# Kernel optimization log

Measured on AMD Instinct MI355X. Metric: run time of the kernel, lower is better.

Reference implementation:

```python
import jax, jax.numpy as jnp
import numpy as np

B, T, C, H = 2, 2048, 1024, 16
D = C // H  # head_dim = 64


def setup_inputs() -> dict:
    key = jax.random.key(0)
    ks = jax.random.split(key, 5)
    s = 1.0 / np.sqrt(C)
    return {
        "x": jax.random.normal(ks[0], (B, T, C), jnp.float32),
        "Wq": jax.random.normal(ks[1], (C, C), jnp.float32) * s,
        "bq": jnp.zeros((C,), jnp.float32),
        "Wk": jax.random.normal(ks[2], (C, C), jnp.float32) * s,
        "bk": jnp.zeros((C,), jnp.float32),
        "Wv": jax.random.normal(ks[3], (C, C), jnp.float32) * s,
        "bv": jnp.zeros((C,), jnp.float32),
        "Wo": jax.random.normal(ks[4], (C, C), jnp.float32) * s,
        "bo": jnp.zeros((C,), jnp.float32),
    }


def reference(x, Wq, bq, Wk, bk, Wv, bv, Wo, bo):
    Bx, Tx, Cx = x.shape
    # torch Linear: y = x @ W.T + b
    q = (x @ Wq.T + bq).reshape(Bx, Tx, H, D).transpose(0, 2, 1, 3)  # [B,H,T,D]
    k = (x @ Wk.T + bk).reshape(Bx, Tx, H, D).transpose(0, 2, 1, 3)
    v = (x @ Wv.T + bv).reshape(Bx, Tx, H, D).transpose(0, 2, 1, 3)
    att = jnp.einsum("bhqd,bhkd->bhqk", q, k) / np.sqrt(D).astype(np.float32)
    mask = jnp.tril(jnp.ones((Tx, Tx), bool))  # causal mask [T,T]
    att = jnp.where(mask, att, -jnp.inf)
    att = jax.nn.softmax(att, axis=-1)
    out = jnp.einsum("bhqk,bhkd->bhqd", att, v)
    out = out.transpose(0, 2, 1, 3).reshape(Bx, Tx, Cx)
    return out @ Wo.T + bo
```

## Files before the change

kernel.cpp:

```cpp
#include <hip/hip_runtime.h>
#include <hip/hip_bf16.h>

#define B_ 2
#define T_ 2048
#define C_ 1024
#define H_ 16
#define D_ 64

typedef unsigned short u16;
typedef __bf16 bf16x8 __attribute__((ext_vector_type(8)));
typedef float floatx4 __attribute__((ext_vector_type(4)));

__device__ __forceinline__ float bf2f(u16 u) {
  union { unsigned int i; float f; } x; x.i = ((unsigned int)u) << 16; return x.f;
}
__device__ __forceinline__ u16 f2bf(float f) {
  union { float f; unsigned int i; } x; x.f = f;
  unsigned int r = x.i + 0x7fffu + ((x.i >> 16) & 1u);
  return (u16)(r >> 16);
}

__device__ __forceinline__ void gld16(void* lds, const void* g) {
  __builtin_amdgcn_global_load_lds(
      (const __attribute__((address_space(1))) unsigned int*)g,
      (__attribute__((address_space(3))) unsigned int*)lds, 16, 0, 0);
}

#define NXF4 1048576
#define NWF4 262144

__global__ __launch_bounds__(256) void cvt_all(
    const float* __restrict__ x,  const float* __restrict__ Wq,
    const float* __restrict__ Wk, const float* __restrict__ Wv,
    const float* __restrict__ Wo, u16* __restrict__ dst_base)
{
  const int i = blockIdx.x * 256 + threadIdx.x;
  const float* src; size_t off;
  if (i < NXF4)               { src = x;  off = i; }
  else if (i < NXF4 + NWF4)   { src = Wq; off = i - NXF4; }
  else if (i < NXF4 + 2*NWF4) { src = Wk; off = i - (NXF4 + NWF4); }
  else if (i < NXF4 + 3*NWF4) { src = Wv; off = i - (NXF4 + 2*NWF4); }
  else                        { src = Wo; off = i - (NXF4 + 3*NWF4); }
  float4 f = ((const float4*)src)[off];
  ushort4 o;
  o.x = f2bf(f.x); o.y = f2bf(f.y); o.z = f2bf(f.z); o.w = f2bf(f.w);
  ((ushort4*)dst_base)[i] = o;
}

#define QSCALE 0.1803368801111f

__global__ __launch_bounds__(256) void gemm_qkv(
    const u16* __restrict__ X, const u16* __restrict__ Wb,
    const float* __restrict__ b0, const float* __restrict__ b1,
    const float* __restrict__ b2,
    u16* __restrict__ Yq, u16* __restrict__ Yk, u16* __restrict__ Yv)
{
  const int K = C_;
  __shared__ __align__(16) u16 As[128 * 32];
  __shared__ __align__(16) u16 Bs[128 * 32];
  __shared__ __align__(16) u16 Es[64 * 128];

  const int tid  = threadIdx.x;
  const int wv   = tid >> 6;
  const int lane = tid & 63;
  const int mcol = lane & 15;
  const int quad = lane >> 4;
  const int wr = wv >> 1, wc = wv & 1;
  const int m0 = blockIdx.x * 128;
  const int n0 = blockIdx.y * 128;
  const int z  = blockIdx.z;

  const u16* W = Wb + (size_t)z * C_ * C_;

  const int srow = tid >> 2;
  const int scol = (tid & 3) * 8;
  const u16* xp0 = X + (size_t)(m0 + srow) * K + scol;
  const u16* xp1 = xp0 + (size_t)64 * K;
  const u16* wp0 = W + (size_t)(n0 + srow) * K + scol;
  const u16* wp1 = wp0 + (size_t)64 * K;

  floatx4 acc[4][4] = {};

  for (int k0 = 0; k0 < K; k0 += 32) {
    gld16(&As[tid * 8],        xp0 + k0);
    gld16(&As[2048 + tid * 8], xp1 + k0);
    gld16(&Bs[tid * 8],        wp0 + k0);
    gld16(&Bs[2048 + tid * 8], wp1 + k0);
    __syncthreads();

    bf16x8 a[4], b[4];
#pragma unroll
    for (int rf = 0; rf < 4; ++rf)
      a[rf] = *(const bf16x8*)&As[(wr * 64 + rf * 16 + mcol) * 32 + quad * 8];
#pragma unroll
    for (int cf = 0; cf < 4; ++cf)
      b[cf] = *(const bf16x8*)&Bs[(wc * 64 + cf * 16 + mcol) * 32 + quad * 8];
#pragma unroll
    for (int rf = 0; rf < 4; ++rf)
#pragma unroll
      for (int cf = 0; cf < 4; ++cf)
        acc[rf][cf] = __builtin_amdgcn_mfma_f32_16x16x32_bf16(
            a[rf], b[cf], acc[rf][cf], 0, 0, 0);
    __syncthreads();
  }

  if (z == 2) {
#pragma unroll
    for (int p = 0; p < 2; ++p) {
      __syncthreads();
      if (wc == p) {
#pragma unroll
        for (int cf = 0; cf < 4; ++cf) {
          const int rn = cf * 16 + mcol;
          const float bv = b2[n0 + p * 64 + rn];
#pragma unroll
          for (int rf = 0; rf < 4; ++rf) {
            const int gm = wr * 8 + rf * 2 + (quad >> 1);
            const int slot = gm ^ (rn & 7);
            ushort4 pk;
            pk.x = f2bf(acc[rf][cf][0] + bv);
            pk.y = f2bf(acc[rf][cf][1] + bv);
            pk.z = f2bf(acc[rf][cf][2] + bv);
            pk.w = f2bf(acc[rf][cf][3] + bv);
            *(ushort4*)&Es[rn * 128 + slot * 8 + (quad & 1) * 4] = pk;
          }
        }
      }
      __syncthreads();
      const int c = tid & 15;
      const int bb = m0 >> 11;
      const int t0 = (m0 & (T_ - 1)) + c * 8;
#pragma unroll
      for (int i = 0; i < 4; ++i) {
        const int rn = (tid >> 4) + i * 16;
        const int slot = c ^ (rn & 7);
        const uint4 val = *(const uint4*)&Es[rn * 128 + slot * 8];
        const int n = n0 + p * 64 + rn;
        const int h = n >> 6, d = n & (D_ - 1);
        *(uint4*)&Yv[(((size_t)bb * H_ + h) * D_ + d) * T_ + t0] = val;
      }
    }
  } else {
    const float* bias = (z == 0 ? b0 : b1);
#pragma unroll
    for (int cf = 0; cf < 4; ++cf) {
      const int n = n0 + wc * 64 + cf * 16 + mcol;
      const float bv = bias[n];
      const int h = n >> 6, d = n & (D_ - 1);
#pragma unroll
      for (int rf = 0; rf < 4; ++rf) {
#pragma unroll
        for (int r = 0; r < 4; ++r) {
          const int m = m0 + wr * 64 + rf * 16 + quad * 4 + r;
          const int bb = m >> 11, t = m & (T_ - 1);
          const float v = acc[rf][cf][r] + bv;
          const size_t idx = (((size_t)bb * H_ + h) * T_ + t) * D_ + d;
          if (z == 0) Yq[idx] = f2bf(v * QSCALE);
          else        Yk[idx] = f2bf(v);
        }
      }
    }
  }
}

__global__ __launch_bounds__(256) void gemm_out(
    const u16* __restrict__ X, const u16* __restrict__ W,
    const float* __restrict__ bias, float* __restrict__ Yf)
{
  const int K = C_, N = C_;
  __shared__ __align__(16) u16 As[128 * 32];
  __shared__ __align__(16) u16 Bs[64 * 32];

  const int tid  = threadIdx.x;
  const int wv   = tid >> 6;
  const int lane = tid & 63;
  const int mcol = lane & 15;
  const int quad = lane >> 4;
  const int wr = wv >> 1, wc = wv & 1;
  const int m0 = blockIdx.x * 128;
  const int n0 = blockIdx.y * 64;

  const int srow = tid >> 2;
  const int scol = (tid & 3) * 8;
  const u16* xp0 = X + (size_t)(m0 + srow) * K + scol;
  const u16* xp1 = xp0 + (size_t)64 * K;
  const u16* wp  = W + (size_t)(n0 + srow) * K + scol;

  floatx4 acc[4][2] = {};

  for (int k0 = 0; k0 < K; k0 += 32) {
    gld16(&As[tid * 8],        xp0 + k0);
    gld16(&As[2048 + tid * 8], xp1 + k0);
    gld16(&Bs[tid * 8],        wp + k0);
    __syncthreads();

    bf16x8 a[4], b[2];
#pragma unroll
    for (int rf = 0; rf < 4; ++rf)
      a[rf] = *(const bf16x8*)&As[(wr * 64 + rf * 16 + mcol) * 32 + quad * 8];
#pragma unroll
    for (int cf = 0; cf < 2; ++cf)
      b[cf] = *(const bf16x8*)&Bs[(wc * 32 + cf * 16 + mcol) * 32 + quad * 8];
#pragma unroll
    for (int rf = 0; rf < 4; ++rf)
#pragma unroll
      for (int cf = 0; cf < 2; ++cf)
        acc[rf][cf] = __builtin_amdgcn_mfma_f32_16x16x32_bf16(
            a[rf], b[cf], acc[rf][cf], 0, 0, 0);
    __syncthreads();
  }

#pragma unroll
  for (int cf = 0; cf < 2; ++cf) {
    const int n = n0 + wc * 32 + cf * 16 + mcol;
    const float bv = bias[n];
#pragma unroll
    for (int rf = 0; rf < 4; ++rf) {
#pragma unroll
      for (int r = 0; r < 4; ++r) {
        const int m = m0 + wr * 64 + rf * 16 + quad * 4 + r;
        Yf[(size_t)m * N + n] = acc[rf][cf][r] + bv;
      }
    }
  }
}

#define KSB 4096
#define VTB 5120

__global__ __launch_bounds__(256) void attn_flash(
    const u16* __restrict__ Q, const u16* __restrict__ K,
    const u16* __restrict__ Vg, u16* __restrict__ O)
{
  __shared__ __align__(16) u16 Ks[2 * KSB];
  __shared__ __align__(16) u16 Vt[2 * VTB];
  __shared__ __align__(16) u16 Ps[4][16 * 72];

  const int tid  = threadIdx.x;
  const int wv   = tid >> 6;
  const int lane = tid & 63;
  const int mcol = lane & 15;
  const int quad = lane >> 4;

  const int bx = blockIdx.x;
  const int bh = bx & 31;
  const int iq = 31 - (bx >> 5);
  const size_t base  = (size_t)bh * T_ * D_;
  const size_t vbase = (size_t)bh * D_ * T_;
  const int b = bh >> 4, h = bh & (H_ - 1);

  for (int idx = tid; idx < 16 * 64; idx += 256) {
    const u16 val = (idx < 64) ? (u16)0x3F80 : (u16)0;
    Vt[64 * 64 + idx]       = val;
    Vt[VTB + 64 * 64 + idx] = val;
  }

  const int srow = lane >> 3;
  const int sg   = (lane & 7) ^ srow;
  const int c0 = wv * 2, c1 = wv * 2 + 1;
  const int sl0 = (quad ^ (mcol & 7)) * 8;

  const int h3 = mcol >> 3, lo = mcol & 7;
  u16* psw = &Ps[wv][0];
  int colsw[4];
#pragma unroll
  for (int nt = 0; nt < 4; ++nt)
    colsw[nt] = (((nt * 2 + h3) ^ quad) * 8) + lo;
  const int g0 = quad ^ (mcol >> 2);

  const size_t koff0 = base + (size_t)(c0 * 8 + srow) * D_ + sg * 8;
  const size_t koff1 = base + (size_t)(c1 * 8 + srow) * D_ + sg * 8;
  const size_t voff0 = vbase + (size_t)(c0 * 8 + srow) * T_ + sg * 8;
  const size_t voff1 = vbase + (size_t)(c1 * 8 + srow) * T_ + sg * 8;

  const u16* qg = Q + base + (size_t)(iq * 64 + wv * 16 + mcol) * D_ + quad * 8;
  const bf16x8 qf0 = *(const bf16x8*)qg;
  const bf16x8 qf1 = *(const bf16x8*)(qg + 32);

  floatx4 oacc[5] = {};

  __syncthreads();
  gld16(&Ks[c0 * 512 + lane * 8], K  + koff0);
  gld16(&Ks[c1 * 512 + lane * 8], K  + koff1);
  gld16(&Vt[c0 * 512 + lane * 8], Vg + voff0);
  gld16(&Vt[c1 * 512 + lane * 8], Vg + voff1);

  for (int j = 0; j <= iq; ++j) {
    const int cur = j & 1;
    __syncthreads();

    if (j < iq) {
      const int nb = cur ^ 1;
      const size_t kj = (size_t)(j + 1) * 64 * D_;
      const int    vj = (j + 1) * 64;
      gld16(&Ks[nb * KSB + c0 * 512 + lane * 8], K  + koff0 + kj);
      gld16(&Ks[nb * KSB + c1 * 512 + lane * 8], K  + koff1 + kj);
      gld16(&Vt[nb * VTB + c0 * 512 + lane * 8], Vg + voff0 + vj);
      gld16(&Vt[nb * VTB + c1 * 512 + lane * 8], Vg + voff1 + vj);
    }

    const u16* ksb = &Ks[cur * KSB];
    const u16* vtb = &Vt[cur * VTB];

    floatx4 sacc[4] = {};
#pragma unroll
    for (int nt = 0; nt < 4; ++nt) {
      const u16* kr = &ksb[(nt * 16 + mcol) * 64];
      bf16x8 kb0 = *(const bf16x8*)&kr[sl0];
      bf16x8 kb1 = *(const bf16x8*)&kr[sl0 ^ 32];
      sacc[nt] = __builtin_amdgcn_mfma_f32_16x16x32_bf16(qf0, kb0, sacc[nt], 0, 0, 0);
      sacc[nt] = __builtin_amdgcn_mfma_f32_16x16x32_bf16(qf1, kb1, sacc[nt], 0, 0, 0);
    }

    if (j == iq) {
#pragma unroll
      for (int nt = 0; nt < 4; ++nt) {
        const int col = nt * 16 + mcol;
#pragma unroll
        for (int r = 0; r < 4; ++r)
          if (col > wv * 16 + quad * 4 + r) sacc[nt][r] = -1e30f;
      }
    }

#pragma unroll
    for (int nt = 0; nt < 4; ++nt)
#pragma unroll
      for (int r = 0; r < 4; ++r) {
        const float p = exp2f(sacc[nt][r]);
        psw[(quad * 4 + r) * 72 + colsw[nt]] =
            (u16)((__float_as_uint(p) + 0x8000u) >> 16);
      }

    __builtin_amdgcn_wave_barrier();

    bf16x8 pa0 = *(const bf16x8*)&psw[mcol * 72 + g0 * 8];
    bf16x8 pa1 = *(const bf16x8*)&psw[mcol * 72 + g0 * 8 + 32];
#pragma unroll
    for (int dt = 0; dt < 5; ++dt) {
      const u16* vr = &vtb[(dt * 16 + mcol) * 64];
      bf16x8 vb0 = *(const bf16x8*)&vr[sl0];
      bf16x8 vb1 = *(const bf16x8*)&vr[sl0 ^ 32];
      oacc[dt] = __builtin_amdgcn_mfma_f32_16x16x32_bf16(pa0, vb0, oacc[dt], 0, 0, 0);
      oacc[dt] = __builtin_amdgcn_mfma_f32_16x16x32_bf16(pa1, vb1, oacc[dt], 0, 0, 0);
    }
  }

  float invl[4];
#pragma unroll
  for (int r = 0; r < 4; ++r)
    invl[r] = 1.f / __shfl(oacc[4][r], lane & 48);
#pragma unroll
  for (int dt = 0; dt < 4; ++dt) {
    const int c = h * D_ + dt * 16 + mcol;
#pragma unroll
    for (int r = 0; r < 4; ++r) {
      const int t = iq * 64 + wv * 16 + quad * 4 + r;
      O[((size_t)b * T_ + t) * C_ + c] = f2bf(oacc[dt][r] * invl[r]);
    }
  }
}

extern "C" void kernel_launch(void* const* d_in, const int* in_sizes, int n_in,
                              void* d_out, int out_size, void* d_ws, size_t ws_size,
                              hipStream_t stream) {
  const float* x  = (const float*)d_in[0];
  const float* Wq = (const float*)d_in[1];
  const float* bq = (const float*)d_in[2];
  const float* Wk = (const float*)d_in[3];
  const float* bk = (const float*)d_in[4];
  const float* Wv = (const float*)d_in[5];
  const float* bv = (const float*)d_in[6];
  const float* Wo = (const float*)d_in[7];
  const float* bo = (const float*)d_in[8];
  float* out = (float*)d_out;

  const size_t NX = (size_t)B_ * T_ * C_;
  const size_t NW = (size_t)C_ * C_;

  u16* xb  = (u16*)d_ws;
  u16* wqb = xb  + NX;
  u16* wkb = wqb + NW;
  u16* wvb = wkb + NW;
  u16* wob = wvb + NW;
  u16* q   = wob + NW;
  u16* k   = q   + NX;
  u16* v   = k   + NX;
  u16* ctx = v   + NX;

  cvt_all<<<dim3((NXF4 + 4 * NWF4) / 256), 256, 0, stream>>>(x, Wq, Wk, Wv, Wo, xb);

  gemm_qkv<<<dim3(32, 8, 3), 256, 0, stream>>>(xb, wqb, bq, bk, bv, q, k, v);

  attn_flash<<<dim3(1024), 256, 0, stream>>>(q, k, v, ctx);

  gemm_out<<<dim3(32, 16), 256, 0, stream>>>(ctx, wob, bo, out);
}
```

Measured before the change: 198.1 us.

## Rewrite QKV GEMM as 256x256 double-buffered 8-wave kernel with XCD-aware tiling

Replaces the 128x128 single-buffered QKV projection GEMM with a 256x256 tile kernel using 8 waves, K-step 64, and double-buffered LDS (128KB). Global loads for upcoming K slices are interleaved with MFMA phases, with split barriers and s_setprio raising MFMA priority. Block indices are remapped so neighbouring tiles land on the same XCD for L2 reuse, and LDS uses an XOR swizzle. The V epilogue now writes 4-element transposed chunks straight to global instead of staging through LDS, which may make stores less coalesced. The large LDS footprint limits how many blocks fit per CU.

New measurement: 187.4 us. 1.06x faster.

```diff
diff --git a/kernel.cpp b/kernel.cpp
--- a/kernel.cpp
+++ b/kernel.cpp
@@ -49,114 +49,189 @@
 
 #define QSCALE 0.1803368801111f
 
-__global__ __launch_bounds__(256) void gemm_qkv(
+#define MFMA16(MH, NH, BREG)                                                  \
+  do {                                                                        \
+    __builtin_amdgcn_s_setprio(1);                                            \
+    _Pragma("unroll")                                                         \
+    for (int f = 0; f < 4; ++f) {                                             \
+      _Pragma("unroll")                                                       \
+      for (int g = 0; g < 2; ++g) {                                           \
+        acc[(MH)*4 + f][(NH)*2 + g] = __builtin_amdgcn_mfma_f32_16x16x32_bf16(\
+            a[f][0], BREG[g][0], acc[(MH)*4 + f][(NH)*2 + g], 0, 0, 0);       \
+        acc[(MH)*4 + f][(NH)*2 + g] = __builtin_amdgcn_mfma_f32_16x16x32_bf16(\
+            a[f][1], BREG[g][1], acc[(MH)*4 + f][(NH)*2 + g], 0, 0, 0);       \
+      }                                                                       \
+    }                                                                         \
+    __builtin_amdgcn_s_setprio(0);                                            \
+  } while (0)
+
+#define PBAR()                                                \
+  do {                                                        \
+    asm volatile("" ::: "memory");                            \
+    __builtin_amdgcn_s_barrier();                             \
+    asm volatile("s_waitcnt lgkmcnt(0)" ::: "memory");        \
+  } while (0)
+
+#define EBAR()                                                \
+  do {                                                        \
+    asm volatile("" ::: "memory");                            \
+    __builtin_amdgcn_s_barrier();                             \
+    asm volatile("" ::: "memory");                            \
+  } while (0)
+
+__global__ __launch_bounds__(512, 2) void gemm_qkv8(
     const u16* __restrict__ X, const u16* __restrict__ Wb,
     const float* __restrict__ b0, const float* __restrict__ b1,
     const float* __restrict__ b2,
     u16* __restrict__ Yq, u16* __restrict__ Yk, u16* __restrict__ Yv)
 {
-  const int K = C_;
-  __shared__ __align__(16) u16 As[128 * 32];
-  __shared__ __align__(16) u16 Bs[128 * 32];
-  __shared__ __align__(16) u16 Es[64 * 128];
+  __shared__ __align__(16) u16 L[65536];
 
   const int tid  = threadIdx.x;
+  const int lane = tid & 63;
+  const int m16  = lane & 15;
+  const int q4   = lane >> 4;
   const int wv   = tid >> 6;
-  const int lane = tid & 63;
-  const int mcol = lane & 15;
-  const int quad = lane >> 4;
-  const int wr = wv >> 1, wc = wv & 1;
-  const int m0 = blockIdx.x * 128;
-  const int n0 = blockIdx.y * 128;
-  const int z  = blockIdx.z;
-
-  const u16* W = Wb + (size_t)z * C_ * C_;
-
-  const int srow = tid >> 2;
-  const int scol = (tid & 3) * 8;
-  const u16* xp0 = X + (size_t)(m0 + srow) * K + scol;
-  const u16* xp1 = xp0 + (size_t)64 * K;
-  const u16* wp0 = W + (size_t)(n0 + srow) * K + scol;
-  const u16* wp1 = wp0 + (size_t)64 * K;
-
-  floatx4 acc[4][4] = {};
-
-  for (int k0 = 0; k0 < K; k0 += 32) {
-    gld16(&As[tid * 8],        xp0 + k0);
-    gld16(&As[2048 + tid * 8], xp1 + k0);
-    gld16(&Bs[tid * 8],        wp0 + k0);
-    gld16(&Bs[2048 + tid * 8], wp1 + k0);
-    __syncthreads();
-
-    bf16x8 a[4], b[4];
-#pragma unroll
-    for (int rf = 0; rf < 4; ++rf)
-      a[rf] = *(const bf16x8*)&As[(wr * 64 + rf * 16 + mcol) * 32 + quad * 8];
-#pragma unroll
-    for (int cf = 0; cf < 4; ++cf)
-      b[cf] = *(const bf16x8*)&Bs[(wc * 64 + cf * 16 + mcol) * 32 + quad * 8];
-#pragma unroll
-    for (int rf = 0; rf < 4; ++rf)
-#pragma unroll
-      for (int cf = 0; cf < 4; ++cf)
-        acc[rf][cf] = __builtin_amdgcn_mfma_f32_16x16x32_bf16(
-            a[rf], b[cf], acc[rf][cf], 0, 0, 0);
-    __syncthreads();
-  }
+  const int wm   = wv >> 2;
+  const int wn   = wv & 3;
+
+  const int bid = blockIdx.x;
+  const int xcd = bid & 7;
+  const int idx = bid >> 3;
+  const int bx  = (xcd & 3) * 4 + (idx & 3);
+  const int by  = (xcd >> 2) * 6 + (idx >> 2);
+
+  const u16* Abase  = X  + (size_t)bx * 256 * C_;
+  const u16* Bbase  = Wb + (size_t)by * 256 * C_;
+  const u16* A1base = Abase + (size_t)128 * C_;
+  const u16* B1base = Bbase + (size_t)128 * C_;
+
+  const int s0 = tid,       r0 = s0 >> 3;
+  const int s1 = tid + 512, r1 = s1 >> 3;
+  const int k0a = ((s0 & 7) ^ (r0 & 7)) * 8;
+  const int k1a = ((s1 & 7) ^ (r1 & 7)) * 8;
+
+#define STAGE(dsthalf, srcrows, kofs)                                         \
+  do {                                                                        \
+    gld16(&(dsthalf)[s0 * 8], (srcrows) + (size_t)r0 * C_ + (kofs) + k0a);    \
+    gld16(&(dsthalf)[s1 * 8], (srcrows) + (size_t)r1 * C_ + (kofs) + k1a);    \
+  } while (0)
+
+  u16* buf0 = L;
+  u16* buf1 = L + 32768;
+
+  STAGE(buf0 + 16384, Bbase, 0);
+  STAGE(buf0,         Abase, 0);
+  STAGE(buf0 + 24576, B1base, 0);
+  STAGE(buf0 + 8192,  A1base, 0);
+  STAGE(buf1 + 16384, Bbase, 64);
+  STAGE(buf1,         Abase, 64);
+  asm volatile("s_waitcnt vmcnt(4)" ::: "memory");
+  __builtin_amdgcn_s_barrier();
+  asm volatile("" ::: "memory");
+
+  floatx4 acc[8][4] = {};
+
+  const int a0off = m16 * 64 + ((q4      ^ (lane & 7)) * 8);
+  const int a1off = m16 * 64 + (((q4 + 4) ^ (lane & 7)) * 8);
+  const int bro   = (wn & 1) * 4096;
+
+  for (int i = 0; i < 16; ++i) {
+    u16* buf  = (i & 1) ? buf1 : buf0;
+    u16* bufn = (i & 1) ? buf0 : buf1;
+    const u16* Ah = buf + wm * 8192;
+    const u16* Bh = buf + 16384 + (wn >> 1) * 8192;
+    const bool p1 = (i + 1) < 16;
+    const bool p2 = (i + 2) < 16;
+    const int  k1 = (i + 1) * 64;
+    const int  k2 = (i + 2) * 64;
+
+    bf16x8 a[4][2], bA[2][2], bB[2][2];
+
+#pragma unroll
+    for (int f = 0; f < 4; ++f) {
+      a[f][0] = *(const bf16x8*)&Ah[f * 1024 + a0off];
+      a[f][1] = *(const bf16x8*)&Ah[f * 1024 + a1off];
+    }
+#pragma unroll
+    for (int g = 0; g < 2; ++g) {
+      bA[g][0] = *(const bf16x8*)&Bh[bro + g * 1024 + a0off];
+      bA[g][1] = *(const bf16x8*)&Bh[bro + g * 1024 + a1off];
+    }
+    if (p1) STAGE(bufn + 24576, B1base, k1);
+    PBAR();
+    MFMA16(0, 0, bA);
+    EBAR();
+
+#pragma unroll
+    for (int g = 0; g < 2; ++g) {
+      bB[g][0] = *(const bf16x8*)&Bh[bro + 2048 + g * 1024 + a0off];
+      bB[g][1] = *(const bf16x8*)&Bh[bro + 2048 + g * 1024 + a1off];
+    }
+    if (p1) STAGE(bufn + 8192, A1base, k1);
+    PBAR();
+    MFMA16(0, 1, bB);
+    EBAR();
+
+#pragma unroll
+    for (int f = 0; f < 4; ++f) {
+      a[f][0] = *(const bf16x8*)&Ah[4096 + f * 1024 + a0off];
+      a[f][1] = *(const bf16x8*)&Ah[4096 + f * 1024 + a1off];
+    }
+    if (p2) STAGE(buf + 16384, Bbase, k2);
+    PBAR();
+    MFMA16(1, 1, bB);
+    EBAR();
+
+    if (p2) STAGE(buf, Abase, k2);
+    PBAR();
+    MFMA16(1, 0, bA);
+    asm volatile("" ::: "memory");
+    if (p2) asm volatile("s_waitcnt vmcnt(4)" ::: "memory");
+    else    asm volatile("s_waitcnt vmcnt(0)" ::: "memory");
+    __builtin_amdgcn_s_barrier();
+    asm volatile("" ::: "memory");
+  }
+
+  const int z    = by >> 2;
+  const int nloc = (by & 3) * 256 + wn * 64;
+  const float* bias = (z == 0) ? b0 : (z == 1) ? b1 : b2;
+  const int mbase = bx * 256 + wm * 128 + q4 * 4;
 
   if (z == 2) {
 #pragma unroll
-    for (int p = 0; p < 2; ++p) {
-      __syncthreads();
-      if (wc == p) {
-#pragma unroll
-        for (int cf = 0; cf < 4; ++cf) {
-          const int rn = cf * 16 + mcol;
-          const float bv = b2[n0 + p * 64 + rn];
-#pragma unroll
-          for (int rf = 0; rf < 4; ++rf) {
-            const int gm = wr * 8 + rf * 2 + (quad >> 1);
-            const int slot = gm ^ (rn & 7);
-            ushort4 pk;
-            pk.x = f2bf(acc[rf][cf][0] + bv);
-            pk.y = f2bf(acc[rf][cf][1] + bv);
-            pk.z = f2bf(acc[rf][cf][2] + bv);
-            pk.w = f2bf(acc[rf][cf][3] + bv);
-            *(ushort4*)&Es[rn * 128 + slot * 8 + (quad & 1) * 4] = pk;
-          }
-        }
+    for (int nf = 0; nf < 4; ++nf) {
+      const int nz = nloc + nf * 16 + m16;
+      const float bv = bias[nz];
+      const int h = nz >> 6, d = nz & (D_ - 1);
+#pragma unroll
+      for (int mf = 0; mf < 8; ++mf) {
+        const int m  = mbase + mf * 16;
+        const int bb = m >> 11, t = m & (T_ - 1);
+        ushort4 pk;
+        pk.x = f2bf(acc[mf][nf][0] + bv);
+        pk.y = f2bf(acc[mf][nf][1] + bv);
+        pk.z = f2bf(acc[mf][nf][2] + bv);
+        pk.w = f2bf(acc[mf][nf][3] + bv);
+        *(ushort4*)&Yv[(((size_t)bb * H_ + h) * D_ + d) * T_ + t] = pk;
       }
-      __syncthreads();
-      const int c = tid & 15;
-      const int bb = m0 >> 11;
-      const int t0 = (m0 & (T_ - 1)) + c * 8;
-#pragma unroll
-      for (int i = 0; i < 4; ++i) {
-        const int rn = (tid >> 4) + i * 16;
-        const int slot = c ^ (rn & 7);
-        const uint4 val = *(const uint4*)&Es[rn * 128 + slot * 8];
-        const int n = n0 + p * 64 + rn;
-        const int h = n >> 6, d = n & (D_ - 1);
-        *(uint4*)&Yv[(((size_t)bb * H_ + h) * D_ + d) * T_ + t0] = val;
-      }
     }
   } else {
-    const float* bias = (z == 0 ? b0 : b1);
-#pragma unroll
-    for (int cf = 0; cf < 4; ++cf) {
-      const int n = n0 + wc * 64 + cf * 16 + mcol;
-      const float bv = bias[n];
-      const int h = n >> 6, d = n & (D_ - 1);
-#pragma unroll
-      for (int rf = 0; rf < 4; ++rf) {
+    u16* Y = z ? Yk : Yq;
+    const float sc = z ? 1.0f : QSCALE;
+#pragma unroll
+    for (int nf = 0; nf < 4; ++nf) {
+      const int nz = nloc + nf * 16 + m16;
+      const float bv = bias[nz];
+      const int h = nz >> 6, d = nz & (D_ - 1);
+#pragma unroll
+      for (int mf = 0; mf < 8; ++mf) {
+        const int m  = mbase + mf * 16;
+        const int bb = m >> 11, tq = m & (T_ - 1);
 #pragma unroll
         for (int r = 0; r < 4; ++r) {
-          const int m = m0 + wr * 64 + rf * 16 + quad * 4 + r;
-          const int bb = m >> 11, t = m & (T_ - 1);
-          const float v = acc[rf][cf][r] + bv;
-          const size_t idx = (((size_t)bb * H_ + h) * T_ + t) * D_ + d;
-          if (z == 0) Yq[idx] = f2bf(v * QSCALE);
-          else        Yk[idx] = f2bf(v);
+          Y[(((size_t)bb * H_ + h) * T_ + (tq + r)) * D_ + d] =
+              f2bf((acc[mf][nf][r] + bv) * sc);
         }
       }
     }
@@ -389,7 +464,7 @@
 
   cvt_all<<<dim3((NXF4 + 4 * NWF4) / 256), 256, 0, stream>>>(x, Wq, Wk, Wv, Wo, xb);
 
-  gemm_qkv<<<dim3(32, 8, 3), 256, 0, stream>>>(xb, wqb, bq, bk, bv, q, k, v);
+  gemm_qkv8<<<dim3(192), 512, 0, stream>>>(xb, wqb, bq, bk, bv, q, k, v);
 
   attn_flash<<<dim3(1024), 256, 0, stream>>>(q, k, v, ctx);
 
```
